# Optimization experiments

Measured on AMD Instinct MI355X. Metric: run time of the kernel, lower is better.

Reference implementation:

```python
import jax, jax.numpy as jnp
import numpy as np

NUM_FORMULAS = 256
NUM_CONJ_ARR = [6, 9, 12, 15]
DEPTH_ARR = [2, 4, 6]
TEMPERATURE = 2.0
INPUT_DIM = 512
BATCH = 8192

# --- static DNF structure (mirrors build-time indicator matrices) ---
_group = NUM_FORMULAS // len(NUM_CONJ_ARR)                       # 64 formulas per group
_conj_per_formula = np.repeat(np.array(NUM_CONJ_ARR), _group)     # [F]
_CONJ2FORM = np.repeat(np.arange(NUM_FORMULAS), _conj_per_formula)  # [C] = 2688
TOTAL_CONJ = int(_CONJ2FORM.shape[0])
_depths = np.tile(np.array(DEPTH_ARR), TOTAL_CONJ // len(DEPTH_ARR))  # depth per conjunction
_LIT2CONJ = np.repeat(np.arange(TOTAL_CONJ), _depths)             # [L] = 10752
TOTAL_LIT = int(_LIT2CONJ.shape[0])


def setup_inputs() -> dict:
    key = jax.random.key(0)
    k = jax.random.split(key, 6)
    x = jax.random.normal(k[0], (BATCH, INPUT_DIM), jnp.float32)
    # literals_random_mask: binary feature-subset mask per literal (build-time constant)
    random_mask = (jax.random.uniform(k[1], (INPUT_DIM, TOTAL_LIT)) < 0.5).astype(jnp.float32)
    glorot = jnp.sqrt(2.0 / (INPUT_DIM + TOTAL_LIT))
    # weight is pre-multiplied by the random mask at build time
    weight = jax.random.normal(k[2], (INPUT_DIM, TOTAL_LIT), jnp.float32) * glorot * random_mask
    # learnable_binary_mask: soft binary-threshold output in [0, 1]
    learnable_binary_mask = jax.random.uniform(k[3], (INPUT_DIM, TOTAL_LIT), jnp.float32)
    bias = jnp.zeros((TOTAL_LIT,), jnp.float32)
    mu = jax.random.normal(k[4], (NUM_FORMULAS, INPUT_DIM), jnp.float32)
    sigma = 1.0 + 0.1 * jax.random.uniform(k[5], (NUM_FORMULAS,), jnp.float32)
    return {
        "x": x, "weight": weight, "learnable_binary_mask": learnable_binary_mask,
        "bias": bias, "mu": mu, "sigma": sigma,
        "lit2conj": jnp.asarray(_LIT2CONJ, jnp.int32),
        "conj2form": jnp.asarray(_CONJ2FORM, jnp.int32),
    }


def reference(x, weight, learnable_binary_mask, bias, mu, sigma, lit2conj, conj2form):
    # literal projection: tanh(x @ (W * M) + b)             -> [B, L]
    literals = jnp.tanh(x @ (weight * learnable_binary_mask) + bias)
    # soft AND over literals of each conjunction: tanh(sum - d + 1.5)
    and_bias = jax.ops.segment_sum(jnp.ones((TOTAL_LIT,), literals.dtype), lit2conj,
                                   num_segments=TOTAL_CONJ)
    conj_sum = jax.ops.segment_sum(literals.T, lit2conj, num_segments=TOTAL_CONJ).T  # [B, C]
    conj = jnp.tanh(conj_sum - and_bias + 1.5)
    # soft OR over conjunctions of each formula: tanh(sum + d - 1.5)
    or_bias = jax.ops.segment_sum(jnp.ones((TOTAL_CONJ,), conj.dtype), conj2form,
                                  num_segments=NUM_FORMULAS)
    form_sum = jax.ops.segment_sum(conj.T, conj2form, num_segments=NUM_FORMULAS).T   # [B, F]
    dnnf = jnp.tanh(form_sum + or_bias - 1.5)
    # localization: softmax over formulas of temperature-scaled RBF, via GEMM expansion
    sq = (jnp.sum(x * x, axis=1, keepdims=True) - 2.0 * (x @ mu.T)
          + jnp.sum(mu * mu, axis=1)[None, :])                                       # [B, F]
    loc = jax.nn.softmax(TEMPERATURE * jnp.exp(-0.5 * sq / (sigma * sigma)[None, :]), axis=-1)
    return dnnf * loc
```

## Files before the change

kernel.cpp:

```cpp
#include <hip/hip_runtime.h>


#define BATCH 8192
#define IDIM 512
#define NFORM 256
#define NLIT 10752
#define WT_ROWS 11136

#define BM 128
#define BN 192
#define BK 64
#define BUFB 40960
#define SLITP 196

typedef __bf16 bf16x8 __attribute__((ext_vector_type(8)));
typedef float f32x4 __attribute__((ext_vector_type(4)));
typedef unsigned short u16;
typedef unsigned int u32;

__device__ __forceinline__ u16 f2bf(float f) {
  u32 u = __float_as_uint(f);
  u = (u + 0x7fffu + ((u >> 16) & 1u)) >> 16;
  return (u16)u;
}

__device__ __forceinline__ float fast_tanh(float x) {
  float e = __expf(2.0f * x);
  return 1.0f - 2.0f * __builtin_amdgcn_rcpf(e + 1.0f);
}

__device__ __forceinline__ void async_cp16(const void* g, void* l) {
  __builtin_amdgcn_global_load_lds(
      (const u32 __attribute__((address_space(1)))*)g,
      (u32 __attribute__((address_space(3)))*)l, 16, 0, 0);
}


#define PREPX_BLKS 2048
#define PREPW_BLKS 1344

__global__ __launch_bounds__(256) void prep_all(
    const float* __restrict__ x, const float* __restrict__ W,
    const float* __restrict__ M, const float* __restrict__ mu,
    u16* __restrict__ xb, u16* __restrict__ wt, float* __restrict__ xsq,
    float* __restrict__ musq, float* __restrict__ form_sum) {
  __shared__ float lds[64 * 65];
  const int blk = blockIdx.x, tid = threadIdx.x;

  if (blk < PREPX_BLKS) {
    ((uint4*)form_sum)[blk * 256 + tid] = make_uint4(0, 0, 0, 0);
    int wave = tid >> 6, lane = tid & 63;
    int row = blk * 4 + wave;
    const float4* px = (const float4*)(x + (size_t)row * IDIM);
    float4 a = px[lane * 2], b = px[lane * 2 + 1];
    uint4 pk;
    pk.x = (u32)f2bf(a.x) | ((u32)f2bf(a.y) << 16);
    pk.y = (u32)f2bf(a.z) | ((u32)f2bf(a.w) << 16);
    pk.z = (u32)f2bf(b.x) | ((u32)f2bf(b.y) << 16);
    pk.w = (u32)f2bf(b.z) | ((u32)f2bf(b.w) << 16);
    ((uint4*)(xb + (size_t)row * IDIM))[lane] = pk;
    float s = a.x * a.x + a.y * a.y + a.z * a.z + a.w * a.w +
              b.x * b.x + b.y * b.y + b.z * b.z + b.w * b.w;
#pragma unroll
    for (int o = 32; o > 0; o >>= 1) s += __shfl_down(s, o);
    if (lane == 0) xsq[row] = s;
  } else if (blk < PREPX_BLKS + PREPW_BLKS) {
    int b = blk - PREPX_BLKS;
    int l0 = (b % 168) * 64, k0 = (b / 168) * 64;
#pragma unroll
    for (int j = 0; j < 4; ++j) {
      int idx = tid + j * 256;
      int kk = idx >> 4, l4 = idx & 15;
      size_t g = (size_t)(k0 + kk) * NLIT + l0 + l4 * 4;
      float4 w4 = *(const float4*)(W + g);
      float4 m4 = *(const float4*)(M + g);
      lds[kk * 65 + l4 * 4 + 0] = w4.x * m4.x;
      lds[kk * 65 + l4 * 4 + 1] = w4.y * m4.y;
      lds[kk * 65 + l4 * 4 + 2] = w4.z * m4.z;
      lds[kk * 65 + l4 * 4 + 3] = w4.w * m4.w;
    }
    __syncthreads();
    int l = tid >> 2, kq = tid & 3;
    u32 pk[8];
#pragma unroll
    for (int t = 0; t < 8; ++t) {
      u16 lo = f2bf(lds[(kq * 16 + 2 * t) * 65 + l]);
      u16 hi = f2bf(lds[(kq * 16 + 2 * t + 1) * 65 + l]);
      pk[t] = (u32)lo | ((u32)hi << 16);
    }
    u32* dst = (u32*)(wt + (size_t)(l0 + l) * IDIM + k0 + kq * 16);
    ((uint4*)dst)[0] = make_uint4(pk[0], pk[1], pk[2], pk[3]);
    ((uint4*)dst)[1] = make_uint4(pk[4], pk[5], pk[6], pk[7]);
  } else {
    int b = blk - PREPX_BLKS - PREPW_BLKS;
    if (b < 256) {
      float s = 0.f;
#pragma unroll
      for (int j = tid; j < IDIM; j += 256) {
        float v = mu[(size_t)b * IDIM + j];
        wt[(size_t)(NLIT + b) * IDIM + j] = f2bf(v);
        s += v * v;
      }
      float* red = lds;
      red[tid] = s;
      __syncthreads();
      for (int sh = 128; sh > 0; sh >>= 1) {
        if (tid < sh) red[tid] += red[tid + sh];
        __syncthreads();
      }
      if (tid == 0) musq[b] = red[0];
    } else {
      int row = NLIT + 256 + (b - 256);
      for (int j = tid; j < IDIM; j += 256) wt[(size_t)row * IDIM + j] = 0;
    }
  }
}


__global__ __launch_bounds__(256, 2) void dnnf_gemm(
    const u16* __restrict__ xb, const u16* __restrict__ wt,
    const float* __restrict__ bias, float* __restrict__ form_sum,
    float* __restrict__ dotbuf) {
  __shared__ __align__(16) char smraw[2 * BUFB];
  float* slit = (float*)smraw;

  const int tid = threadIdx.x;
  const int wave = tid >> 6, lane = tid & 63;
  const int wm = wave & 1, wn = wave >> 1;
  const int m0 = blockIdx.y * BM, n0 = blockIdx.x * BN;
  const int q = lane >> 4, cn = lane & 15;

  const int kg8 = ((tid & 7) ^ ((tid >> 3) & 7)) * 8;
  const u16* pa = xb + (size_t)(m0 + (tid >> 3)) * IDIM + kg8;
  const u16* pb = wt + (size_t)(n0 + (tid >> 3)) * IDIM + kg8;
  const int dA = tid * 16;
  const int dB = 16384 + tid * 16;

  const int kg0_16 = ((q ^ (cn & 7)) << 4);
  int offA[4], offB[6];
#pragma unroll
  for (int mf = 0; mf < 4; ++mf)
    offA[mf] = (wm * 64 + mf * 16 + cn) * 128 + kg0_16;
#pragma unroll
  for (int nf = 0; nf < 6; ++nf)
    offB[nf] = 16384 + (wn * 96 + nf * 16 + cn) * 128 + kg0_16;

  f32x4 acc[4][6];
#pragma unroll
  for (int a = 0; a < 4; ++a)
#pragma unroll
    for (int b = 0; b < 6; ++b) acc[a][b] = (f32x4){0.f, 0.f, 0.f, 0.f};

#pragma unroll
  for (int i = 0; i < 4; ++i)
    async_cp16(pa + (size_t)i * 32 * IDIM, smraw + dA + i * 4096);
#pragma unroll
  for (int i = 0; i < 6; ++i)
    async_cp16(pb + (size_t)i * 32 * IDIM, smraw + dB + i * 4096);
  pa += BK;
  pb += BK;

#pragma unroll
  for (int kt = 0; kt < 8; ++kt) {
    const char* bufc = smraw + (kt & 1) * BUFB;
    if (kt < 7) {
      char* bufn = smraw + ((kt + 1) & 1) * BUFB;
#pragma unroll
      for (int i = 0; i < 4; ++i)
        async_cp16(pa + (size_t)i * 32 * IDIM, bufn + dA + i * 4096);
#pragma unroll
      for (int i = 0; i < 6; ++i)
        async_cp16(pb + (size_t)i * 32 * IDIM, bufn + dB + i * 4096);
      pa += BK;
      pb += BK;
      asm volatile("s_waitcnt vmcnt(10)\n\ts_barrier" ::: "memory");
    } else {
      asm volatile("s_waitcnt vmcnt(0)\n\ts_barrier" ::: "memory");
    }
#pragma unroll
    for (int ks = 0; ks < 2; ++ks) {
      const int x64 = ks ? 64 : 0;
      bf16x8 af[4], bfr[6];
#pragma unroll
      for (int mf = 0; mf < 4; ++mf)
        af[mf] = *(const bf16x8*)(bufc + (offA[mf] ^ x64));
#pragma unroll
      for (int nf = 0; nf < 6; ++nf)
        bfr[nf] = *(const bf16x8*)(bufc + (offB[nf] ^ x64));
#pragma unroll
      for (int mf = 0; mf < 4; ++mf)
#pragma unroll
        for (int nf = 0; nf < 6; ++nf)
          acc[mf][nf] = __builtin_amdgcn_mfma_f32_16x16x32_bf16(
              af[mf], bfr[nf], acc[mf][nf], 0, 0, 0);
    }
    if (kt < 7)
      asm volatile("s_waitcnt lgkmcnt(0)\n\ts_barrier" ::: "memory");
  }
  __syncthreads();

  if (n0 < NLIT) {
    float bv[6];
#pragma unroll
    for (int nf = 0; nf < 6; ++nf) bv[nf] = bias[n0 + wn * 96 + nf * 16 + cn];

#pragma unroll
    for (int ph = 0; ph < 2; ++ph) {
      if (ph) __syncthreads();
      if (wm == ph) {
#pragma unroll
        for (int nf = 0; nf < 6; ++nf) {
          int col = wn * 96 + nf * 16 + cn;
#pragma unroll
          for (int mf = 0; mf < 4; ++mf)
#pragma unroll
            for (int reg = 0; reg < 4; ++reg) {
              int lr = mf * 16 + q * 4 + reg;
              slit[lr * SLITP + col] = fast_tanh(acc[mf][nf][reg] + bv[nf]);
            }
        }
      }
      __syncthreads();

      int r = tid >> 2, sub = tid & 3;
      const float* lrow = slit + r * SLITP + sub * 48;
      int c0 = ((n0 + sub * 48) / 12) * 3;
      size_t grow = (size_t)(m0 + ph * 64 + r) * NFORM;
      float run = 0.f;
      int fprev = -1;
#pragma unroll
      for (int tr = 0; tr < 4; ++tr) {
        const float* p = lrow + tr * 12;
        float s2 = p[0] + p[1];
        float s4 = p[2] + p[3] + p[4] + p[5];
        float s6 = p[6] + p[7] + p[8] + p[9] + p[10] + p[11];
        float v = fast_tanh(s2 - 0.5f) + fast_tanh(s4 - 2.5f) +
                  fast_tanh(s6 - 4.5f);
        int c = c0 + tr * 3;
        int f = (c < 384)    ? (c / 6)
                : (c < 960)  ? 64 + (c - 384) / 9
                : (c < 1728) ? 128 + (c - 960) / 12
                             : 192 + (c - 1728) / 15;
        if (f != fprev) {
          if (fprev >= 0) atomicAdd(form_sum + grow + fprev, run);
          fprev = f;
          run = 0.f;
        }
        run += v;
      }
      atomicAdd(form_sum + grow + fprev, run);
    }
  } else {
#pragma unroll
    for (int nf = 0; nf < 6; ++nf) {
      int col = n0 - NLIT + wn * 96 + nf * 16 + cn;
      if (col < NFORM) {
#pragma unroll
        for (int mf = 0; mf < 4; ++mf)
#pragma unroll
          for (int reg = 0; reg < 4; ++reg) {
            int row = wm * 64 + mf * 16 + q * 4 + reg;
            dotbuf[(size_t)(m0 + row) * NFORM + col] = acc[mf][nf][reg];
          }
      }
    }
  }
}


__global__ __launch_bounds__(256) void finale(
    const float* __restrict__ form_sum, const float* __restrict__ dotbuf,
    const float* __restrict__ xsq, const float* __restrict__ musq,
    const float* __restrict__ sigma, float* __restrict__ out) {
  int wave = threadIdx.x >> 6, lane = threadIdx.x & 63;
  int r = blockIdx.x * 4 + wave;
  size_t base = (size_t)r * NFORM;
  float xs = xsq[r];
  float e[4], s = 0.f;
#pragma unroll
  for (int j = 0; j < 4; ++j) {
    int f = j * 64 + lane;
    float sq = xs - 2.0f * dotbuf[base + f] + musq[f];
    float sg = sigma[f];
    float p = __expf(-0.5f * sq / (sg * sg));
    e[j] = __expf(2.0f * p);
    s += e[j];
  }
#pragma unroll
  for (int o = 32; o > 0; o >>= 1) s += __shfl_xor(s, o);
  float inv = __builtin_amdgcn_rcpf(s);
#pragma unroll
  for (int j = 0; j < 4; ++j) {
    int f = j * 64 + lane;
    float dn = fast_tanh(form_sum[base + f] + (float)(6 + 3 * j) - 1.5f);
    out[base + f] = dn * e[j] * inv;
  }
}


extern "C" void kernel_launch(void* const* d_in, const int* in_sizes, int n_in,
                              void* d_out, int out_size, void* d_ws,
                              size_t ws_size, hipStream_t stream) {
  const float* x = (const float*)d_in[0];
  const float* W = (const float*)d_in[1];
  const float* M = (const float*)d_in[2];
  const float* bias = (const float*)d_in[3];
  const float* mu = (const float*)d_in[4];
  const float* sigma = (const float*)d_in[5];
  float* out = (float*)d_out;

  float* form_sum = (float*)d_ws;
  float* dotbuf = form_sum + (size_t)BATCH * NFORM;
  u16* xb = (u16*)(dotbuf + (size_t)BATCH * NFORM);
  u16* wt = xb + (size_t)BATCH * IDIM;
  float* xsq = (float*)(wt + (size_t)WT_ROWS * IDIM);
  float* musq = xsq + BATCH;

  prep_all<<<PREPX_BLKS + PREPW_BLKS + 384, 256, 0, stream>>>(
      x, W, M, mu, xb, wt, xsq, musq, form_sum);
  dnnf_gemm<<<dim3(WT_ROWS / BN, BATCH / BM), 256, 0, stream>>>(xb, wt, bias,
                                                                form_sum, dotbuf);
  finale<<<BATCH / 4, 256, 0, stream>>>(form_sum, dotbuf, xsq, musq, sigma, out);
}
```

Measured before the change: 245.2 us.

## Use per-wave bf16-packed transposed LDS staging for the literal epilogue

The epilogue now stages tanh'd literals in a per-wave, column-major LDS region, packed as bf16 pairs, instead of a shared fp32 row-major tile. This removes the two-phase block-wide barriers, and each lane reduces two rows at once. It also halves the LDS footprint and traffic. In exchange, literal values are rounded to bf16 before the conjunction sums, which costs some accuracy.

```diff
diff --git a/kernel.cpp b/kernel.cpp
--- a/kernel.cpp
+++ b/kernel.cpp
@@ -11,7 +11,7 @@
 #define BN 192
 #define BK 64
 #define BUFB 40960
-#define SLITP 196
+#define PADU 36
 
 typedef __bf16 bf16x8 __attribute__((ext_vector_type(8)));
 typedef float f32x4 __attribute__((ext_vector_type(4)));
@@ -122,7 +122,6 @@
     const float* __restrict__ bias, float* __restrict__ form_sum,
     float* __restrict__ dotbuf) {
   __shared__ __align__(16) char smraw[2 * BUFB];
-  float* slit = (float*)smraw;
 
   const int tid = threadIdx.x;
   const int wave = tid >> 6, lane = tid & 63;
@@ -200,56 +199,73 @@
   __syncthreads();
 
   if (n0 < NLIT) {
-    float bv[6];
-#pragma unroll
-    for (int nf = 0; nf < 6; ++nf) bv[nf] = bias[n0 + wn * 96 + nf * 16 + cn];
-
-#pragma unroll
-    for (int ph = 0; ph < 2; ++ph) {
-      if (ph) __syncthreads();
-      if (wm == ph) {
-#pragma unroll
-        for (int nf = 0; nf < 6; ++nf) {
-          int col = wn * 96 + nf * 16 + cn;
-#pragma unroll
-          for (int mf = 0; mf < 4; ++mf)
-#pragma unroll
-            for (int reg = 0; reg < 4; ++reg) {
-              int lr = mf * 16 + q * 4 + reg;
-              slit[lr * SLITP + col] = fast_tanh(acc[mf][nf][reg] + bv[nf]);
-            }
+    u32* wbase = (u32*)smraw + wave * 96 * PADU;
+
+#pragma unroll
+    for (int nf = 0; nf < 6; ++nf) {
+      float bv = bias[n0 + wn * 96 + nf * 16 + cn];
+      int col = nf * 16 + cn;
+#pragma unroll
+      for (int mf = 0; mf < 4; ++mf) {
+        float t0 = fast_tanh(acc[mf][nf][0] + bv);
+        float t1 = fast_tanh(acc[mf][nf][1] + bv);
+        float t2 = fast_tanh(acc[mf][nf][2] + bv);
+        float t3 = fast_tanh(acc[mf][nf][3] + bv);
+        uint2 pk;
+        pk.x = (u32)f2bf(t0) | ((u32)f2bf(t1) << 16);
+        pk.y = (u32)f2bf(t2) | ((u32)f2bf(t3) << 16);
+        *(uint2*)(wbase + col * PADU + mf * 8 + q * 2) = pk;
+      }
+    }
+
+    int rp = lane >> 1, half = lane & 1;
+    const u32* src = wbase + half * 48 * PADU + rp;
+    int gr = m0 + wm * 64 + rp * 2;
+    float* fs0 = form_sum + (size_t)gr * NFORM;
+    float* fs1 = fs0 + NFORM;
+    int cbase = ((n0 + wn * 96 + half * 48) / 12) * 3;
+    float run0 = 0.f, run1 = 0.f;
+    int fprev = -1;
+#define LOF(u) __uint_as_float((u) << 16)
+#define HIF(u) __uint_as_float((u) & 0xffff0000u)
+#pragma unroll
+    for (int tr = 0; tr < 4; ++tr) {
+      const u32* p = src + tr * 12 * PADU;
+      u32 a0 = p[0], a1 = p[PADU], a2 = p[2 * PADU], a3 = p[3 * PADU];
+      u32 a4 = p[4 * PADU], a5 = p[5 * PADU], a6 = p[6 * PADU];
+      u32 a7 = p[7 * PADU], a8 = p[8 * PADU], a9 = p[9 * PADU];
+      u32 a10 = p[10 * PADU], a11 = p[11 * PADU];
+      float s2l = LOF(a0) + LOF(a1);
+      float s2h = HIF(a0) + HIF(a1);
+      float s4l = LOF(a2) + LOF(a3) + LOF(a4) + LOF(a5);
+      float s4h = HIF(a2) + HIF(a3) + HIF(a4) + HIF(a5);
+      float s6l = LOF(a6) + LOF(a7) + LOF(a8) + LOF(a9) + LOF(a10) + LOF(a11);
+      float s6h = HIF(a6) + HIF(a7) + HIF(a8) + HIF(a9) + HIF(a10) + HIF(a11);
+      float v0 = fast_tanh(s2l - 0.5f) + fast_tanh(s4l - 2.5f) +
+                 fast_tanh(s6l - 4.5f);
+      float v1 = fast_tanh(s2h - 0.5f) + fast_tanh(s4h - 2.5f) +
+                 fast_tanh(s6h - 4.5f);
+      int c = cbase + tr * 3;
+      int f = (c < 384)    ? (c / 6)
+              : (c < 960)  ? 64 + (c - 384) / 9
+              : (c < 1728) ? 128 + (c - 960) / 12
+                           : 192 + (c - 1728) / 15;
+      if (f != fprev) {
+        if (fprev >= 0) {
+          atomicAdd(fs0 + fprev, run0);
+          atomicAdd(fs1 + fprev, run1);
         }
-      }
-      __syncthreads();
-
-      int r = tid >> 2, sub = tid & 3;
-      const float* lrow = slit + r * SLITP + sub * 48;
-      int c0 = ((n0 + sub * 48) / 12) * 3;
-      size_t grow = (size_t)(m0 + ph * 64 + r) * NFORM;
-      float run = 0.f;
-      int fprev = -1;
-#pragma unroll
-      for (int tr = 0; tr < 4; ++tr) {
-        const float* p = lrow + tr * 12;
-        float s2 = p[0] + p[1];
-        float s4 = p[2] + p[3] + p[4] + p[5];
-        float s6 = p[6] + p[7] + p[8] + p[9] + p[10] + p[11];
-        float v = fast_tanh(s2 - 0.5f) + fast_tanh(s4 - 2.5f) +
-                  fast_tanh(s6 - 4.5f);
-        int c = c0 + tr * 3;
-        int f = (c < 384)    ? (c / 6)
-                : (c < 960)  ? 64 + (c - 384) / 9
-                : (c < 1728) ? 128 + (c - 960) / 12
-                             : 192 + (c - 1728) / 15;
-        if (f != fprev) {
-          if (fprev >= 0) atomicAdd(form_sum + grow + fprev, run);
-          fprev = f;
-          run = 0.f;
-        }
-        run += v;
-      }
-      atomicAdd(form_sum + grow + fprev, run);
-    }
+        fprev = f;
+        run0 = 0.f;
+        run1 = 0.f;
+      }
+      run0 += v0;
+      run1 += v1;
+    }
+    atomicAdd(fs0 + fprev, run0);
+    atomicAdd(fs1 + fprev, run1);
+#undef LOF
+#undef HIF
   } else {
 #pragma unroll
     for (int nf = 0; nf < 6; ++nf) {
```

Measured after the change: 256.8 us. 4.8% more time.

## Load A-operand fragments directly from global into registers, staging only B in LDS

Applied to the files above, without the earlier changes.

The x (A) tile is no longer staged through shared memory. Each wave loads its MFMA A fragments straight from global memory into a double-buffered register array, one K-tile ahead. Only the weight (B) tile still goes through LDS, which shrinks the per-buffer LDS footprint and removes the A-side LDS reads. In exchange it uses more VGPRs, issues uncoalesced 16-byte global loads that are duplicated across the waves sharing an M slice, and relies on a tuned vmcnt count being correct.

```diff
diff --git a/kernel.cpp b/kernel.cpp
--- a/kernel.cpp
+++ b/kernel.cpp
@@ -10,7 +10,7 @@
 #define BM 128
 #define BN 192
 #define BK 64
-#define BUFB 40960
+#define BUFB 24576
 #define SLITP 196
 
 typedef __bf16 bf16x8 __attribute__((ext_vector_type(8)));
@@ -121,7 +121,7 @@
     const u16* __restrict__ xb, const u16* __restrict__ wt,
     const float* __restrict__ bias, float* __restrict__ form_sum,
     float* __restrict__ dotbuf) {
-  __shared__ __align__(16) char smraw[2 * BUFB];
+  __shared__ __align__(16) char smraw[64 * SLITP * 4];
   float* slit = (float*)smraw;
 
   const int tid = threadIdx.x;
@@ -131,19 +131,16 @@
   const int q = lane >> 4, cn = lane & 15;
 
   const int kg8 = ((tid & 7) ^ ((tid >> 3) & 7)) * 8;
-  const u16* pa = xb + (size_t)(m0 + (tid >> 3)) * IDIM + kg8;
   const u16* pb = wt + (size_t)(n0 + (tid >> 3)) * IDIM + kg8;
-  const int dA = tid * 16;
-  const int dB = 16384 + tid * 16;
+  const int dB = tid * 16;
+
+  const u16* pA = xb + (size_t)(m0 + wm * 64 + cn) * IDIM + q * 8;
 
   const int kg0_16 = ((q ^ (cn & 7)) << 4);
-  int offA[4], offB[6];
-#pragma unroll
-  for (int mf = 0; mf < 4; ++mf)
-    offA[mf] = (wm * 64 + mf * 16 + cn) * 128 + kg0_16;
+  int offB[6];
 #pragma unroll
   for (int nf = 0; nf < 6; ++nf)
-    offB[nf] = 16384 + (wn * 96 + nf * 16 + cn) * 128 + kg0_16;
+    offB[nf] = (wn * 96 + nf * 16 + cn) * 128 + kg0_16;
 
   f32x4 acc[4][6];
 #pragma unroll
@@ -151,14 +148,16 @@
 #pragma unroll
     for (int b = 0; b < 6; ++b) acc[a][b] = (f32x4){0.f, 0.f, 0.f, 0.f};
 
-#pragma unroll
-  for (int i = 0; i < 4; ++i)
-    async_cp16(pa + (size_t)i * 32 * IDIM, smraw + dA + i * 4096);
+  bf16x8 af[2][2][4];
 #pragma unroll
   for (int i = 0; i < 6; ++i)
     async_cp16(pb + (size_t)i * 32 * IDIM, smraw + dB + i * 4096);
-  pa += BK;
-  pb += BK;
+#pragma unroll
+  for (int ks = 0; ks < 2; ++ks)
+#pragma unroll
+    for (int mf = 0; mf < 4; ++mf)
+      af[0][ks][mf] =
+          *(const bf16x8*)(pA + (size_t)mf * 16 * IDIM + ks * 32);
 
 #pragma unroll
   for (int kt = 0; kt < 8; ++kt) {
@@ -166,24 +165,24 @@
     if (kt < 7) {
       char* bufn = smraw + ((kt + 1) & 1) * BUFB;
 #pragma unroll
-      for (int i = 0; i < 4; ++i)
-        async_cp16(pa + (size_t)i * 32 * IDIM, bufn + dA + i * 4096);
-#pragma unroll
       for (int i = 0; i < 6; ++i)
-        async_cp16(pb + (size_t)i * 32 * IDIM, bufn + dB + i * 4096);
-      pa += BK;
-      pb += BK;
-      asm volatile("s_waitcnt vmcnt(10)\n\ts_barrier" ::: "memory");
+        async_cp16(pb + (size_t)(kt + 1) * BK + (size_t)i * 32 * IDIM,
+                   bufn + dB + i * 4096);
+#pragma unroll
+      for (int ks = 0; ks < 2; ++ks)
+#pragma unroll
+        for (int mf = 0; mf < 4; ++mf)
+          af[(kt + 1) & 1][ks][mf] =
+              *(const bf16x8*)(pA + (size_t)mf * 16 * IDIM +
+                               (kt + 1) * BK + ks * 32);
+      asm volatile("s_waitcnt vmcnt(14)\n\ts_barrier" ::: "memory");
     } else {
       asm volatile("s_waitcnt vmcnt(0)\n\ts_barrier" ::: "memory");
     }
 #pragma unroll
     for (int ks = 0; ks < 2; ++ks) {
       const int x64 = ks ? 64 : 0;
-      bf16x8 af[4], bfr[6];
-#pragma unroll
-      for (int mf = 0; mf < 4; ++mf)
-        af[mf] = *(const bf16x8*)(bufc + (offA[mf] ^ x64));
+      bf16x8 bfr[6];
 #pragma unroll
       for (int nf = 0; nf < 6; ++nf)
         bfr[nf] = *(const bf16x8*)(bufc + (offB[nf] ^ x64));
@@ -192,7 +191,7 @@
 #pragma unroll
         for (int nf = 0; nf < 6; ++nf)
           acc[mf][nf] = __builtin_amdgcn_mfma_f32_16x16x32_bf16(
-              af[mf], bfr[nf], acc[mf][nf], 0, 0, 0);
+              af[kt & 1][ks][mf], bfr[nf], acc[mf][nf], 0, 0, 0);
     }
     if (kt < 7)
       asm volatile("s_waitcnt lgkmcnt(0)\n\ts_barrier" ::: "memory");
```

Measured after the change: 284.4 us. +16.0%, slower.
